# Performance work log

Measured on AMD Instinct MI355X. Metric: run time of the kernel, lower is better.

## Reference

```python
import jax, jax.numpy as jnp
import numpy as np
import math

NSEG = 4
SAMPLE_RATE = 16  # curve samples per bezier segment
SHARPNESS = 150.0


def _control_radians():
    n = NSEG
    theta = math.pi * 2 / (4 * n) + math.atan(math.tan(2 * math.pi / (4 * n)) / 3)
    r = []
    for i in range(n):
        r += [2 * math.pi / n * i, 2 * math.pi / n * i + theta, 2 * math.pi / n * (i + 1) - theta]
    return jnp.asarray(np.asarray(r, dtype=np.float32).reshape(n, 3))


def sdf_extruded_bezier(quaternion, translation, points, control_polygon, bez_weights, height):
    # quaternion [B,K,4], translation [B,K,3], points [B,M,3],
    # control_polygon [B,K,nseg,3,2], bez_weights [B,K,nseg,2], height [B,K]
    B, K, _ = quaternion.shape
    p = points[:, :, None, :] - translation[:, None, :, :]            # [B,M,K,3]
    q = quaternion[:, None, :, :]
    qn = q / jnp.sqrt(jnp.sum(q * q, -1, keepdims=True) + 1e-8)
    w, qv = qn[..., :1], -qn[..., 1:]                                  # conjugate -> world->local
    t2 = 2.0 * jnp.cross(qv, p)
    pl = p + w * t2 + jnp.cross(qv, t2)                                # local coords [B,M,K,3]
    p2d, pz = pl[..., :2], pl[..., 2]
    # rational cubic bezier per segment: P0,P1,P2 from this segment, P3 = next segment's P0
    P0 = control_polygon[:, :, :, 0, :]
    P1 = control_polygon[:, :, :, 1, :]
    P2 = control_polygon[:, :, :, 2, :]
    P3 = jnp.roll(P0, -1, axis=2)
    ts = jnp.linspace(0.0, 1.0, SAMPLE_RATE, endpoint=False)           # [S]
    b0 = (1 - ts) ** 3
    b1 = 3 * (1 - ts) ** 2 * ts
    b2 = 3 * (1 - ts) * ts ** 2
    b3 = ts ** 3
    w1 = bez_weights[..., 0:1]                                          # [B,K,nseg,1]
    w2 = bez_weights[..., 1:2]
    den = b0 + w1 * b1 + w2 * b2 + b3                                   # [B,K,nseg,S]
    num = (P0[..., None, :] * b0[:, None]
           + P1[..., None, :] * (w1[..., None] * b1[:, None])
           + P2[..., None, :] * (w2[..., None] * b2[:, None])
           + P3[..., None, :] * b3[:, None])                            # [B,K,nseg,S,2]
    curve = (num / den[..., None]).reshape(B, K, NSEG * SAMPLE_RATE, 2)
    rel = curve[:, None] - p2d[..., None, :]                            # [B,M,K,S*nseg,2]
    d2 = jnp.sum(rel * rel, -1)
    dmin = jnp.sqrt(jnp.min(d2, -1) + 1e-12)                            # unsigned 2D distance
    nxt = jnp.roll(rel, -1, axis=-2)
    cross = rel[..., 0] * nxt[..., 1] - rel[..., 1] * nxt[..., 0]
    dot = jnp.sum(rel * nxt, -1)
    winding = jnp.sum(jnp.arctan2(cross, dot), -1) / (2 * math.pi)
    sdf2d = jnp.where(jnp.abs(winding) > 0.5, -dmin, dmin)
    dz = jnp.abs(pz) - jnp.abs(height)[:, None, :]
    sdf = (jnp.minimum(jnp.maximum(sdf2d, dz), 0.0)
           + jnp.sqrt(jnp.maximum(sdf2d, 0.0) ** 2 + jnp.maximum(dz, 0.0) ** 2 + 1e-12))
    return sdf, dmin


def setup_inputs() -> dict:
    key = jax.random.key(0)
    k1, k2, k3, k4 = jax.random.split(key, 4)
    B, M, K, C = 4, 2048, 64, 64
    P = 4 + 3 + 1 + NSEG * 3 + NSEG * 2  # 28
    return {
        "sample_point_coordinates": jax.random.uniform(k1, (B, M, 3), jnp.float32, -1.0, 1.0),
        "primitive_parameters": 0.3 * jax.random.normal(k2, (B, P, K), jnp.float32),
        "intersection_layer_weights": jax.random.uniform(k3, (B, K, C), jnp.float32),
        "union_layer_weights": jax.random.uniform(k4, (B, C), jnp.float32),
        "is_training": 1,
    }


def reference(sample_point_coordinates, primitive_parameters, intersection_layer_weights, union_layer_weights, is_training):
    pp = jnp.swapaxes(primitive_parameters, 1, 2)                       # [B,K,P]
    B, K, _ = pp.shape
    quaternion = pp[..., :4]
    translation = pp[..., 4:7]
    height = pp[..., 7]
    radius = jnp.abs(pp[..., 8:8 + NSEG * 3]).reshape(B, K, NSEG, 3)
    rad = _control_radians()[None, None]                                # [1,1,nseg,3]
    control_polygon = jnp.stack([jnp.cos(rad) * radius, jnp.sin(rad) * radius], -1)
    bez_weights = jnp.abs(pp[..., 8 + NSEG * 3:]).reshape(B, K, NSEG, 2)
    primitive_sdf, support_distances = sdf_extruded_bezier(
        quaternion, translation, sample_point_coordinates, control_polygon, bez_weights, height)
    primitive_occ = jax.nn.sigmoid(-primitive_sdf * SHARPNESS)          # [B,M,K]
    # occupancy_pre_intersection = w*occ + (1-w)*1 = 1 - w*(1-occ), fused
    w_int = intersection_layer_weights[:, None]                         # [B,1,K,C]
    pre_i = 1.0 - w_int * (1.0 - primitive_occ[..., None])              # [B,M,K,C]
    if is_training:
        sw = jax.lax.stop_gradient(jax.nn.softmax(pre_i * -40.0, axis=-2))
        inter = jnp.sum(sw * pre_i, -2)                                 # soft-min -> [B,M,C]
    else:
        inter = jnp.min(pre_i, -2)
    pre_u = union_layer_weights[:, None, :] * inter
    if is_training:
        sw2 = jax.lax.stop_gradient(jax.nn.softmax(pre_u * 40.0, axis=-1))
        occupancies = jnp.sum(sw2 * pre_u, -1)                          # soft-max -> [B,M]
    else:
        occupancies = jnp.max(pre_u, -1)
    return occupancies, primitive_sdf, inter, support_distances
```

## Files before the change

### kernel.cpp

```cpp
#include <hip/hip_runtime.h>
#include <math.h>


#define NB 4
#define NM 2048
#define NK 64
#define NC 64
#define NS 64
#define PPB 4

#define OCC_OFF   0
#define SDF_OFF   8192
#define INTER_OFF 532480
#define SUP_OFF   1056768

#define CT 0.86285621096f
#define ST 0.50544946275f

#define L2E_40  57.70780163555852f
#define L2E_150 216.40425613334447f

__global__ __launch_bounds__(256) void extrude_net_fused(
    const float* __restrict__ pts,
    const float* __restrict__ pp,
    const float* __restrict__ Wint,
    const float* __restrict__ Uw,
    float* __restrict__ out)
{
    __shared__ __align__(16) float4 s_curve4[NS / 2][NK];

    const int tid  = threadIdx.x;
    const int lane = tid & 63;
    const int wv   = tid >> 6;
    const int gpt  = blockIdx.x * PPB + wv;
    const int b    = gpt >> 11;
    const float* __restrict__ ppb = pp + b * (28 * NK);
    const int k = lane;

    {
        const int seg = wv;
        const float r0 = fabsf(ppb[(8 + seg * 3 + 0) * NK + k]);
        const float r1 = fabsf(ppb[(8 + seg * 3 + 1) * NK + k]);
        const float r2 = fabsf(ppb[(8 + seg * 3 + 2) * NK + k]);
        const float rn = fabsf(ppb[(8 + ((seg + 1) & 3) * 3 + 0) * NK + k]);
        const float w1 = fabsf(ppb[(20 + seg * 2 + 0) * NK + k]);
        const float w2 = fabsf(ppb[(20 + seg * 2 + 1) * NK + k]);

        const float cosv = (seg == 0) ? 1.f : (seg == 2) ? -1.f : 0.f;
        const float sinv = (seg == 1) ? 1.f : (seg == 3) ? -1.f : 0.f;
        const float P0x =  r0 * cosv,            P0y = r0 * sinv;
        const float P1x = (CT * cosv - ST * sinv) * r1, P1y = (CT * sinv + ST * cosv) * r1;
        const float P2x = (ST * cosv - CT * sinv) * r2, P2y = (ST * sinv + CT * cosv) * r2;
        const float P3x = -rn * sinv,            P3y = rn * cosv;

        #pragma unroll
        for (int j = 0; j < 16; j += 2) {
            float sx[2], sy[2];
            #pragma unroll
            for (int h = 0; h < 2; ++h) {
                const float t  = (float)(j + h) * 0.0625f;
                const float u  = 1.f - t;
                const float b0 = u * u * u;
                const float b1 = 3.f * u * u * t;
                const float b2 = 3.f * u * t * t;
                const float b3 = t * t * t;
                const float wb1 = w1 * b1, wb2 = w2 * b2;
                const float inv = __builtin_amdgcn_rcpf(b0 + wb1 + wb2 + b3);
                sx[h] = (P0x * b0 + P1x * wb1 + P2x * wb2 + P3x * b3) * inv;
                sy[h] = (P0y * b0 + P1y * wb1 + P2y * wb2 + P3y * b3) * inv;
            }
            s_curve4[seg * 8 + (j >> 1)][k] = make_float4(sx[0], sy[0], sx[1], sy[1]);
        }
    }
    __syncthreads();

    const float ptx = pts[gpt * 3 + 0];
    const float pty = pts[gpt * 3 + 1];
    const float ptz = pts[gpt * 3 + 2];
    float om;
    {
        const float q0 = ppb[0 * NK + k], q1 = ppb[1 * NK + k];
        const float q2 = ppb[2 * NK + k], q3 = ppb[3 * NK + k];
        const float trx = ppb[4 * NK + k], try_ = ppb[5 * NK + k], trz = ppb[6 * NK + k];
        const float h   = ppb[7 * NK + k];

        const float px = ptx - trx, py = pty - try_, pz = ptz - trz;
        const float inv = __builtin_amdgcn_rsqf(q0 * q0 + q1 * q1 + q2 * q2 + q3 * q3 + 1e-8f);
        const float w  = q0 * inv;
        const float vx = -q1 * inv, vy = -q2 * inv, vz = -q3 * inv;
        const float t2x = 2.f * (vy * pz - vz * py);
        const float t2y = 2.f * (vz * px - vx * pz);
        const float t2z = 2.f * (vx * py - vy * px);
        const float plx = px + w * t2x + (vy * t2z - vz * t2y);
        const float ply = py + w * t2y + (vz * t2x - vx * t2z);
        const float plz = pz + w * t2z + (vx * t2y - vy * t2x);

        const float4* __restrict__ col = &s_curve4[0][k];

        const float4 c0 = col[0];
        const float ax = c0.x - plx, ay = c0.y - ply;
        float rx = c0.z - plx, ry = c0.w - ply;
        const bool pos0 = ay > 0.f;
        bool apos = ry > 0.f;
        int wn = 0;
        {
            const float cr = ax * ry - ay * rx;
            wn += ((!pos0) & apos & (cr > 0.f)) ? 1 : 0;
            wn -= (pos0 & (!apos) & (cr < 0.f)) ? 1 : 0;
        }
        float d2a = ax * ax + ay * ay;
        float d2b = rx * rx + ry * ry;
        #pragma unroll
        for (int s2 = 1; s2 < 32; ++s2) {
            const float4 cn = col[s2 * NK];
            const float nx0 = cn.x - plx, ny0 = cn.y - ply;
            const float nx1 = cn.z - plx, ny1 = cn.w - ply;
            const bool b0p = ny0 > 0.f;
            const bool b1p = ny1 > 0.f;
            const float cr0 = rx * ny0 - ry * nx0;
            const float cr1 = nx0 * ny1 - ny0 * nx1;
            wn += ((!apos) & b0p & (cr0 > 0.f)) ? 1 : 0;
            wn -= (apos & (!b0p) & (cr0 < 0.f)) ? 1 : 0;
            wn += ((!b0p) & b1p & (cr1 > 0.f)) ? 1 : 0;
            wn -= (b0p & (!b1p) & (cr1 < 0.f)) ? 1 : 0;
            d2a = fminf(d2a, nx0 * nx0 + ny0 * ny0);
            d2b = fminf(d2b, nx1 * nx1 + ny1 * ny1);
            apos = b1p; rx = nx1; ry = ny1;
        }
        {
            const float cr = rx * ay - ry * ax;
            wn += ((!apos) & pos0 & (cr > 0.f)) ? 1 : 0;
            wn -= (apos & (!pos0) & (cr < 0.f)) ? 1 : 0;
        }
        const float dmin  = sqrtf(fminf(d2a, d2b) + 1e-12f);
        const float sdf2d = (wn != 0) ? -dmin : dmin;
        const float dz    = fabsf(plz) - fabsf(h);
        const float mx    = fmaxf(sdf2d, dz);
        const float e1    = fmaxf(sdf2d, 0.f);
        const float e2    = fmaxf(dz, 0.f);
        const float sdf   = fminf(mx, 0.f) + sqrtf(e1 * e1 + e2 * e2 + 1e-12f);

        out[SDF_OFF + gpt * NK + k] = sdf;
        out[SUP_OFF + gpt * NK + k] = dmin;
        om = __builtin_amdgcn_rcpf(1.f + exp2f(-sdf * L2E_150));
    }
    __syncthreads();

    {
        const float4* __restrict__ wsrc = (const float4*)(Wint + b * (NK * NC));
        float4* wdst = (float4*)&s_curve4[0][0];
        #pragma unroll
        for (int i = 0; i < 4; ++i)
            wdst[i * 256 + tid] = wsrc[i * 256 + tid];
    }
    __syncthreads();

    {
        const int c = lane;
        const float* __restrict__ WbL = (const float*)&s_curve4[0][0];
        float srun = 0.f, trun = 0.f;
        #pragma unroll
        for (int kk = 0; kk < NK; ++kk) {
            const float omk = __shfl(om, kk, 64);
            const float pre = fmaf(-WbL[kk * NC + c], omk, 1.f);
            const float e   = exp2f(pre * -L2E_40);
            srun += e;
            trun = fmaf(e, pre, trun);
        }
        const float inter = trun * __builtin_amdgcn_rcpf(srun);
        out[INTER_OFF + gpt * NC + c] = inter;

        const float pu = Uw[b * NC + c] * inter;
        float umax = pu;
        #pragma unroll
        for (int off = 32; off > 0; off >>= 1)
            umax = fmaxf(umax, __shfl_xor(umax, off, 64));
        const float e = exp2f((pu - umax) * L2E_40);
        float s1 = e, s2 = e * pu;
        #pragma unroll
        for (int off = 32; off > 0; off >>= 1) {
            s1 += __shfl_xor(s1, off, 64);
            s2 += __shfl_xor(s2, off, 64);
        }
        if (lane == 0) out[OCC_OFF + gpt] = s2 * __builtin_amdgcn_rcpf(s1);
    }
}

extern "C" void kernel_launch(void* const* d_in, const int* in_sizes, int n_in,
                              void* d_out, int out_size, void* d_ws, size_t ws_size,
                              hipStream_t stream) {
    const float* pts  = (const float*)d_in[0];
    const float* pp   = (const float*)d_in[1];
    const float* Wint = (const float*)d_in[2];
    const float* Uw   = (const float*)d_in[3];
    float* out = (float*)d_out;
    (void)d_ws; (void)ws_size;

    const int grid = (NB * NM) / PPB;
    extrude_net_fused<<<grid, 256, 0, stream>>>(pts, pp, Wint, Uw, out);
}
```

Measured before the change: 88.78 us.

## Double points per block, split curve build across waves, broadcast occupancy via LDS

Each block now handles eight points with 512 threads, so the per-block curve sampling and the Wint load into LDS are amortized over twice as many points, and each wave computes only half of one segment's samples. The point load moves ahead of the first barrier, and the curve-column reads are software-prefetched two float4 entries ahead. Per-lane occupancy is written to a small LDS array and read back as float4, replacing 64 cross-lane shuffles. The cost is more LDS per block and a tighter register budget from launch_bounds(512,8), which could cause spills or lower occupancy.

```diff
diff --git a/kernel.cpp b/kernel.cpp
--- a/kernel.cpp
+++ b/kernel.cpp
@@ -7,7 +7,7 @@
 #define NK 64
 #define NC 64
 #define NS 64
-#define PPB 4
+#define PPB 8
 
 #define OCC_OFF   0
 #define SDF_OFF   8192
@@ -20,7 +20,7 @@
 #define L2E_40  57.70780163555852f
 #define L2E_150 216.40425613334447f
 
-__global__ __launch_bounds__(256) void extrude_net_fused(
+__global__ __launch_bounds__(512, 8) void extrude_net_fused(
     const float* __restrict__ pts,
     const float* __restrict__ pp,
     const float* __restrict__ Wint,
@@ -28,6 +28,7 @@
     float* __restrict__ out)
 {
     __shared__ __align__(16) float4 s_curve4[NS / 2][NK];
+    __shared__ __align__(16) float  s_om[PPB][NK];
 
     const int tid  = threadIdx.x;
     const int lane = tid & 63;
@@ -37,8 +38,13 @@
     const float* __restrict__ ppb = pp + b * (28 * NK);
     const int k = lane;
 
-    {
-        const int seg = wv;
+    const float ptx = pts[gpt * 3 + 0];
+    const float pty = pts[gpt * 3 + 1];
+    const float ptz = pts[gpt * 3 + 2];
+
+    {
+        const int seg = wv & 3;
+        const int jb  = (wv >> 2) * 8;
         const float r0 = fabsf(ppb[(8 + seg * 3 + 0) * NK + k]);
         const float r1 = fabsf(ppb[(8 + seg * 3 + 1) * NK + k]);
         const float r2 = fabsf(ppb[(8 + seg * 3 + 2) * NK + k]);
@@ -48,13 +54,14 @@
 
         const float cosv = (seg == 0) ? 1.f : (seg == 2) ? -1.f : 0.f;
         const float sinv = (seg == 1) ? 1.f : (seg == 3) ? -1.f : 0.f;
-        const float P0x =  r0 * cosv,            P0y = r0 * sinv;
+        const float P0x =  r0 * cosv,                   P0y = r0 * sinv;
         const float P1x = (CT * cosv - ST * sinv) * r1, P1y = (CT * sinv + ST * cosv) * r1;
         const float P2x = (ST * cosv - CT * sinv) * r2, P2y = (ST * sinv + CT * cosv) * r2;
-        const float P3x = -rn * sinv,            P3y = rn * cosv;
-
-        #pragma unroll
-        for (int j = 0; j < 16; j += 2) {
+        const float P3x = -rn * sinv,                   P3y = rn * cosv;
+
+        #pragma unroll
+        for (int j0 = 0; j0 < 8; j0 += 2) {
+            const int j = jb + j0;
             float sx[2], sy[2];
             #pragma unroll
             for (int h = 0; h < 2; ++h) {
@@ -74,10 +81,6 @@
     }
     __syncthreads();
 
-    const float ptx = pts[gpt * 3 + 0];
-    const float pty = pts[gpt * 3 + 1];
-    const float ptz = pts[gpt * 3 + 2];
-    float om;
     {
         const float q0 = ppb[0 * NK + k], q1 = ppb[1 * NK + k];
         const float q2 = ppb[2 * NK + k], q3 = ppb[3 * NK + k];
@@ -94,12 +97,16 @@
         const float plx = px + w * t2x + (vy * t2z - vz * t2y);
         const float ply = py + w * t2y + (vz * t2x - vx * t2z);
         const float plz = pz + w * t2z + (vx * t2y - vy * t2x);
+        const float dz  = fabsf(plz) - fabsf(h);
 
         const float4* __restrict__ col = &s_curve4[0][k];
 
-        const float4 c0 = col[0];
-        const float ax = c0.x - plx, ay = c0.y - ply;
-        float rx = c0.z - plx, ry = c0.w - ply;
+        const float4 c0v = col[0];
+        float4 cA = col[1 * NK];
+        float4 cB = col[2 * NK];
+
+        const float ax = c0v.x - plx, ay = c0v.y - ply;
+        float rx = c0v.z - plx, ry = c0v.w - ply;
         const bool pos0 = ay > 0.f;
         bool apos = ry > 0.f;
         int wn = 0;
@@ -110,9 +117,8 @@
         }
         float d2a = ax * ax + ay * ay;
         float d2b = rx * rx + ry * ry;
-        #pragma unroll
-        for (int s2 = 1; s2 < 32; ++s2) {
-            const float4 cn = col[s2 * NK];
+
+        auto PROC = [&](const float4 cn) {
             const float nx0 = cn.x - plx, ny0 = cn.y - ply;
             const float nx1 = cn.z - plx, ny1 = cn.w - ply;
             const bool b0p = ny0 > 0.f;
@@ -126,7 +132,19 @@
             d2a = fminf(d2a, nx0 * nx0 + ny0 * ny0);
             d2b = fminf(d2b, nx1 * nx1 + ny1 * ny1);
             apos = b1p; rx = nx1; ry = ny1;
-        }
+        };
+
+        #pragma unroll
+        for (int s2 = 1; s2 <= 29; s2 += 2) {
+            float4 cC = cA, cD = cB;
+            if (s2 + 2 < 32) cC = col[(s2 + 2) * NK];
+            if (s2 + 3 < 32) cD = col[(s2 + 3) * NK];
+            PROC(cA);
+            PROC(cB);
+            cA = cC; cB = cD;
+        }
+        PROC(cA);
+
         {
             const float cr = rx * ay - ry * ax;
             wn += ((!apos) & pos0 & (cr > 0.f)) ? 1 : 0;
@@ -134,7 +152,6 @@
         }
         const float dmin  = sqrtf(fminf(d2a, d2b) + 1e-12f);
         const float sdf2d = (wn != 0) ? -dmin : dmin;
-        const float dz    = fabsf(plz) - fabsf(h);
         const float mx    = fmaxf(sdf2d, dz);
         const float e1    = fmaxf(sdf2d, 0.f);
         const float e2    = fmaxf(dz, 0.f);
@@ -142,7 +159,7 @@
 
         out[SDF_OFF + gpt * NK + k] = sdf;
         out[SUP_OFF + gpt * NK + k] = dmin;
-        om = __builtin_amdgcn_rcpf(1.f + exp2f(-sdf * L2E_150));
+        s_om[wv][k] = __builtin_amdgcn_rcpf(1.f + exp2f(-sdf * L2E_150));
     }
     __syncthreads();
 
@@ -150,22 +167,29 @@
         const float4* __restrict__ wsrc = (const float4*)(Wint + b * (NK * NC));
         float4* wdst = (float4*)&s_curve4[0][0];
         #pragma unroll
-        for (int i = 0; i < 4; ++i)
-            wdst[i * 256 + tid] = wsrc[i * 256 + tid];
+        for (int i = 0; i < 2; ++i)
+            wdst[i * 512 + tid] = wsrc[i * 512 + tid];
     }
     __syncthreads();
 
     {
         const int c = lane;
-        const float* __restrict__ WbL = (const float*)&s_curve4[0][0];
+        const float*  __restrict__ WbL  = (const float*)&s_curve4[0][0];
+        const float4* __restrict__ om4p = (const float4*)&s_om[wv][0];
         float srun = 0.f, trun = 0.f;
-        #pragma unroll
-        for (int kk = 0; kk < NK; ++kk) {
-            const float omk = __shfl(om, kk, 64);
+        auto ACC = [&](float omk, int kk) {
             const float pre = fmaf(-WbL[kk * NC + c], omk, 1.f);
             const float e   = exp2f(pre * -L2E_40);
             srun += e;
             trun = fmaf(e, pre, trun);
+        };
+        #pragma unroll
+        for (int kq = 0; kq < 16; ++kq) {
+            const float4 om4 = om4p[kq];
+            ACC(om4.x, 4 * kq + 0);
+            ACC(om4.y, 4 * kq + 1);
+            ACC(om4.z, 4 * kq + 2);
+            ACC(om4.w, 4 * kq + 3);
         }
         const float inter = trun * __builtin_amdgcn_rcpf(srun);
         out[INTER_OFF + gpt * NC + c] = inter;
@@ -197,5 +221,5 @@
     (void)d_ws; (void)ws_size;
 
     const int grid = (NB * NM) / PPB;
-    extrude_net_fused<<<grid, 256, 0, stream>>>(pts, pp, Wint, Uw, out);
+    extrude_net_fused<<<grid, 512, 0, stream>>>(pts, pp, Wint, Uw, out);
 }
```

After: 88.04 us. No clear change (-0.8%).
